# Performance work log

Measured on AMD Instinct MI355X. Metric: run time of the kernel, lower is better.

The kernel has to match this reference:

```python
import jax, jax.numpy as jnp
import numpy as np

ALPHA = 0.2  # LeakyReLU negative slope


def setup_inputs() -> dict:
    key = jax.random.key(0)
    k1, k2, k3, k4 = jax.random.split(key, 4)
    B, N, F_IN, F_OUT = 8, 2048, 512, 256
    h = jax.random.normal(k1, (B, N, F_IN), dtype=jnp.float32)
    # torch nn.Linear weights: [out, in]
    W = jax.random.normal(k2, (F_OUT, F_IN), dtype=jnp.float32) * (1.414 / np.sqrt(F_IN))
    a1 = jax.random.normal(k3, (1, F_OUT), dtype=jnp.float32) * (1.414 / np.sqrt(F_OUT))
    a2 = jax.random.normal(k4, (1, F_OUT), dtype=jnp.float32) * (1.414 / np.sqrt(F_OUT))
    return {"h": h, "W": W, "a1": a1, "a2": a2}


def reference(h, W, a1, a2):
    # Wh: [B, N, F_out]
    Wh = jnp.einsum('bnf,of->bno', h, W)
    # additive attention scores
    s1 = jnp.einsum('bno,o->bn', Wh, a1[0])  # [B, N]
    s2 = jnp.einsum('bno,o->bn', Wh, a2[0])  # [B, N]
    e = s1[:, :, None] + s2[:, None, :]       # [B, N, N]
    e = jnp.where(e > 0, e, ALPHA * e)         # LeakyReLU
    attention = jax.nn.softmax(e, axis=2)      # softmax over last dim
    # dropout p=0.0 -> identity
    h_prime = jnp.einsum('bnm,bmo->bno', attention, Wh)
    return jax.nn.elu(h_prime)  # concat=True path
```

## Files before the change

### kernel.cpp

```cpp
#include <hip/hip_runtime.h>

typedef __attribute__((ext_vector_type(8))) _Float16 half8;
typedef __attribute__((ext_vector_type(4))) _Float16 half4;
typedef __attribute__((ext_vector_type(4))) float f32x4;
#if __has_builtin(__builtin_amdgcn_cvt_pkrtz)
typedef __attribute__((ext_vector_type(2))) __fp16 fp16x2;
#endif

#define ALPHA 0.2f
#define LOG2E 1.44269504f

__device__ __forceinline__ void gload_lds16(const void* g, void* l) {
  __builtin_amdgcn_global_load_lds((const __attribute__((address_space(1))) unsigned int*)g,
                                   (__attribute__((address_space(3))) unsigned int*)l, 16, 0, 0);
}

__device__ __forceinline__ float fexp2(float x) {
#if __has_builtin(__builtin_amdgcn_exp2f)
  return __builtin_amdgcn_exp2f(x);
#else
  return exp2f(x);
#endif
}

__global__ __launch_bounds__(256) void k_convW(const float* __restrict__ W,
                                               _Float16* __restrict__ W16) {
  int idx4 = blockIdx.x * 256 + threadIdx.x;
  int n = idx4 >> 7;
  int q = idx4 & 127;
  float4 v = *reinterpret_cast<const float4*>(W + n * 512 + q * 4);
  half4 hv = {(_Float16)v.x, (_Float16)v.y, (_Float16)v.z, (_Float16)v.w};
  int kp = (q * 4) ^ ((n & 7) << 3);
  *reinterpret_cast<half4*>(W16 + n * 512 + kp) = hv;
}

__global__ __launch_bounds__(256) void k_uvec(const float* __restrict__ W,
                                              const float* __restrict__ a1,
                                              const float* __restrict__ a2,
                                              float* __restrict__ u1,
                                              float* __restrict__ u2) {
  __shared__ float p1[4][64], p2[4][64];
  int t = threadIdx.x;
  int l = t & 63, g = t >> 6;
  int k = blockIdx.x * 64 + l;
  float x1 = 0.f, x2 = 0.f;
  for (int o = g * 64; o < g * 64 + 64; ++o) {
    float wv = W[o * 512 + k];
    x1 += wv * a1[o];
    x2 += wv * a2[o];
  }
  p1[g][l] = x1; p2[g][l] = x2;
  __syncthreads();
  if (g == 0) {
    u1[k] = p1[0][l] + p1[1][l] + p1[2][l] + p1[3][l];
    u2[k] = p2[0][l] + p2[1][l] + p2[2][l] + p2[3][l];
  }
}

__global__ __launch_bounds__(512) void k_gemm_wh(const float* __restrict__ h,
                                                 const _Float16* __restrict__ W16,
                                                 const float* __restrict__ u1,
                                                 const float* __restrict__ u2,
                                                 float* __restrict__ s1o,
                                                 float* __restrict__ s2o,
                                                 _Float16* __restrict__ WhT) {
  __shared__ _Float16 Ab[2][64 * 64];
  __shared__ _Float16 Bb[3][256 * 64];
  __shared__ float u_lds[1024];
  const int t = threadIdx.x, lane = t & 63, w = t >> 6;
  const int rg = w >> 2, cg = w & 3;
  const int i0 = blockIdx.x * 64;
  const int b = i0 >> 11, n0 = i0 & 2047;
  const int ar = t >> 3, au = t & 7;
  const int arow = lane & 15;
  const float* hrow = h + (size_t)(i0 + ar) * 512 + au * 8;
  const int awoff = ar * 128 + ((au * 16) ^ ((ar & 7) << 4));

  u_lds[t] = u1[t];
  u_lds[512 + t] = u2[t];
  __syncthreads();

  f32x4 acc[2][4];
#pragma unroll
  for (int mi = 0; mi < 2; ++mi)
#pragma unroll
    for (int ni = 0; ni < 4; ++ni) acc[mi][ni] = (f32x4){0.f, 0.f, 0.f, 0.f};
  float x1 = 0.f, x2 = 0.f;

  float4 aRx[2], aRy[2];
  aRx[0] = *reinterpret_cast<const float4*>(hrow);
  aRy[0] = *reinterpret_cast<const float4*>(hrow + 4);
#pragma unroll
  for (int x = 0; x < 2; ++x)
#pragma unroll
    for (int q = 0; q < 4; ++q) {
      int idx = q * 512 + t;
      int cl = idx >> 3, uu = idx & 7;
      gload_lds16(W16 + cl * 512 + x * 64 + uu * 8, (char*)&Bb[x][0] + idx * 16);
    }
  aRx[1] = *reinterpret_cast<const float4*>(hrow + 64);
  aRy[1] = *reinterpret_cast<const float4*>(hrow + 68);
  {
    float4 a0 = aRx[0], a1v = aRy[0];
    half8 av;
    av[0] = (_Float16)a0.x; av[1] = (_Float16)a0.y; av[2] = (_Float16)a0.z; av[3] = (_Float16)a0.w;
    av[4] = (_Float16)a1v.x; av[5] = (_Float16)a1v.y; av[6] = (_Float16)a1v.z; av[7] = (_Float16)a1v.w;
    *reinterpret_cast<half8*>((char*)&Ab[0][0] + awoff) = av;
    const float* up1 = &u_lds[au * 8];
    const float* up2 = &u_lds[512 + au * 8];
    x1 += a0.x * up1[0] + a0.y * up1[1] + a0.z * up1[2] + a0.w * up1[3]
        + a1v.x * up1[4] + a1v.y * up1[5] + a1v.z * up1[6] + a1v.w * up1[7];
    x2 += a0.x * up2[0] + a0.y * up2[1] + a0.z * up2[2] + a0.w * up2[3]
        + a1v.x * up2[4] + a1v.y * up2[5] + a1v.z * up2[6] + a1v.w * up2[7];
  }

#pragma unroll
  for (int kt = 0; kt < 8; ++kt) {
    asm volatile("s_waitcnt vmcnt(6) lgkmcnt(0)" ::: "memory");
    __builtin_amdgcn_s_barrier();
    if (kt < 6) {
      const int k0 = (kt + 2) * 64;
      const int p = (kt + 2) % 3;
#pragma unroll
      for (int q = 0; q < 4; ++q) {
        int idx = q * 512 + t;
        int cl = idx >> 3, uu = idx & 7;
        gload_lds16(W16 + cl * 512 + k0 + uu * 8, (char*)&Bb[p][0] + idx * 16);
      }
      aRx[kt & 1] = *reinterpret_cast<const float4*>(hrow + k0);
      aRy[kt & 1] = *reinterpret_cast<const float4*>(hrow + k0 + 4);
    }
    if (kt < 7) {
      float4 a0 = aRx[(kt + 1) & 1], a1v = aRy[(kt + 1) & 1];
      half8 av;
      av[0] = (_Float16)a0.x; av[1] = (_Float16)a0.y; av[2] = (_Float16)a0.z; av[3] = (_Float16)a0.w;
      av[4] = (_Float16)a1v.x; av[5] = (_Float16)a1v.y; av[6] = (_Float16)a1v.z; av[7] = (_Float16)a1v.w;
      *reinterpret_cast<half8*>((char*)&Ab[(kt + 1) & 1][0] + awoff) = av;
      const float* up1 = &u_lds[(kt + 1) * 64 + au * 8];
      const float* up2 = &u_lds[512 + (kt + 1) * 64 + au * 8];
      x1 += a0.x * up1[0] + a0.y * up1[1] + a0.z * up1[2] + a0.w * up1[3]
          + a1v.x * up1[4] + a1v.y * up1[5] + a1v.z * up1[6] + a1v.w * up1[7];
      x2 += a0.x * up2[0] + a0.y * up2[1] + a0.z * up2[2] + a0.w * up2[3]
          + a1v.x * up2[4] + a1v.y * up2[5] + a1v.z * up2[6] + a1v.w * up2[7];
    }
    const char* Ac = (const char*)&Ab[kt & 1][0];
    const char* Bc = (const char*)&Bb[kt % 3][0];
#pragma unroll
    for (int kk = 0; kk < 2; ++kk) {
      const int jb = ((lane >> 4) * 8 + kk * 32) * 2;
      half8 afr[2];
#pragma unroll
      for (int mi = 0; mi < 2; ++mi) {
        int rr = rg * 32 + 16 * mi + arow;
        afr[mi] = *reinterpret_cast<const half8*>(Ac + rr * 128 + (jb ^ ((rr & 7) << 4)));
      }
#pragma unroll
      for (int ni = 0; ni < 4; ++ni) {
        int nn = cg * 64 + 16 * ni + arow;
        half8 bfr = *reinterpret_cast<const half8*>(Bc + nn * 128 + (jb ^ ((nn & 7) << 4)));
#pragma unroll
        for (int mi = 0; mi < 2; ++mi)
          acc[mi][ni] = __builtin_amdgcn_mfma_f32_16x16x32_f16(afr[mi], bfr, acc[mi][ni], 0, 0, 0);
      }
    }
  }
  x1 += __shfl_xor(x1, 1); x1 += __shfl_xor(x1, 2); x1 += __shfl_xor(x1, 4);
  x2 += __shfl_xor(x2, 1); x2 += __shfl_xor(x2, 2); x2 += __shfl_xor(x2, 4);
  if (au == 0) { s1o[i0 + ar] = x1; s2o[i0 + ar] = x2; }
  _Float16* whtb = WhT + (size_t)b * 256 * 2048;
#pragma unroll
  for (int mi = 0; mi < 2; ++mi)
#pragma unroll
    for (int ni = 0; ni < 4; ++ni) {
      int c = cg * 64 + 16 * ni + arow;
      int nb = n0 + rg * 32 + 16 * mi + (lane >> 4) * 4;
      int np = nb ^ ((c & 7) << 3);
      f32x4 a = acc[mi][ni];
      half4 hv = {(_Float16)a[0], (_Float16)a[1], (_Float16)a[2], (_Float16)a[3]};
      *reinterpret_cast<half4*>(whtb + (size_t)c * 2048 + np) = hv;
    }
}

__global__ __launch_bounds__(1024) void k_attn(const _Float16* __restrict__ WhT,
                                               const float* __restrict__ s1,
                                               const float* __restrict__ s2,
                                               float* __restrict__ out) {
  __shared__ _Float16 Bb[3][256 * 64];
  __shared__ _Float16 Pb[2][64 * 64];
  __shared__ float s2s[2048];
  __shared__ float red[16];
  __shared__ float d_lds[64];
  const int t = threadIdx.x, lane = t & 63, w = t >> 6;
  const int rg = w >> 2, cg = w & 3;
  const int b = blockIdx.x & 7;
  const int i0 = (blockIdx.x >> 3) * 64;
  const _Float16* whtb = WhT + (size_t)b * 256 * 2048;
  const int arow = lane & 15;
  const int pr = t >> 4, pj = t & 15;
  const float s1v = s1[b * 2048 + i0 + pr];

  float2 sv2 = *reinterpret_cast<const float2*>(s2 + b * 2048 + t * 2);
  float m0 = fmaxf(sv2.x, sv2.y);
  *reinterpret_cast<float2*>(&s2s[t * 2]) = make_float2(sv2.x * LOG2E, sv2.y * LOG2E);
#pragma unroll
  for (int off = 32; off >= 1; off >>= 1) m0 = fmaxf(m0, __shfl_xor(m0, off));
  if (lane == 0) red[w] = m0;
  __syncthreads();
  float smaxL;
  {
    float mm = red[0];
#pragma unroll
    for (int i = 1; i < 16; ++i) mm = fmaxf(mm, red[i]);
    smaxL = mm * LOG2E;
  }
  const float s1L = LOG2E * s1v;
  const float e0L = s1L + smaxL;
  const float mrowL = fmaxf(e0L, ALPHA * e0L);
  const float C1 = s1L - mrowL;
  const float C2 = fmaf(ALPHA, s1L, -mrowL);
  const int pwoff = pr * 128 + ((pj * 8) ^ ((pr & 7) << 4));
  half8 onesb;
  {
    _Float16 ov = (arow == 0) ? (_Float16)1.0f : (_Float16)0.0f;
#pragma unroll
    for (int x = 0; x < 8; ++x) onesb[x] = ov;
  }
  f32x4 acc[4];
#pragma unroll
  for (int ni = 0; ni < 4; ++ni) acc[ni] = (f32x4){0.f, 0.f, 0.f, 0.f};
  f32x4 accd = (f32x4){0.f, 0.f, 0.f, 0.f};

  {
    float4 sv = *reinterpret_cast<const float4*>(&s2s[pj * 4]);
    float p0 = fexp2(fmaxf(C1 + sv.x, fmaf(ALPHA, sv.x, C2)));
    float p1 = fexp2(fmaxf(C1 + sv.y, fmaf(ALPHA, sv.y, C2)));
    float p2 = fexp2(fmaxf(C1 + sv.z, fmaf(ALPHA, sv.z, C2)));
    float p3 = fexp2(fmaxf(C1 + sv.w, fmaf(ALPHA, sv.w, C2)));
    half4 hv;
#if __has_builtin(__builtin_amdgcn_cvt_pkrtz)
    fp16x2 q0 = __builtin_amdgcn_cvt_pkrtz(p0, p1);
    fp16x2 q1 = __builtin_amdgcn_cvt_pkrtz(p2, p3);
    hv[0] = (_Float16)q0[0]; hv[1] = (_Float16)q0[1];
    hv[2] = (_Float16)q1[0]; hv[3] = (_Float16)q1[1];
#else
    hv[0] = (_Float16)p0; hv[1] = (_Float16)p1; hv[2] = (_Float16)p2; hv[3] = (_Float16)p3;
#endif
    *reinterpret_cast<half4*>((char*)&Pb[0][0] + pwoff) = hv;
  }
#pragma unroll
  for (int x = 0; x < 2; ++x)
#pragma unroll
    for (int q = 0; q < 2; ++q) {
      int idx = q * 1024 + t;
      int cl = idx >> 3, uu = idx & 7;
      gload_lds16(whtb + (size_t)cl * 2048 + x * 64 + uu * 8, (char*)&Bb[x][0] + idx * 16);
    }

  for (int jt = 0; jt < 32; ++jt) {
    if (jt < 31) asm volatile("s_waitcnt vmcnt(2) lgkmcnt(0)" ::: "memory");
    else         asm volatile("s_waitcnt vmcnt(0) lgkmcnt(0)" ::: "memory");
    __builtin_amdgcn_s_barrier();
    if (jt < 30) {
      const int j0n = (jt + 2) * 64;
      const int p = (jt + 2) % 3;
#pragma unroll
      for (int q = 0; q < 2; ++q) {
        int idx = q * 1024 + t;
        int cl = idx >> 3, uu = idx & 7;
        gload_lds16(whtb + (size_t)cl * 2048 + j0n + uu * 8, (char*)&Bb[p][0] + idx * 16);
      }
    }
    if (jt < 31) {
      float4 sv = *reinterpret_cast<const float4*>(&s2s[(jt + 1) * 64 + pj * 4]);
      float p0 = fexp2(fmaxf(C1 + sv.x, fmaf(ALPHA, sv.x, C2)));
      float p1 = fexp2(fmaxf(C1 + sv.y, fmaf(ALPHA, sv.y, C2)));
      float p2 = fexp2(fmaxf(C1 + sv.z, fmaf(ALPHA, sv.z, C2)));
      float p3 = fexp2(fmaxf(C1 + sv.w, fmaf(ALPHA, sv.w, C2)));
      half4 hv;
#if __has_builtin(__builtin_amdgcn_cvt_pkrtz)
      fp16x2 q0 = __builtin_amdgcn_cvt_pkrtz(p0, p1);
      fp16x2 q1 = __builtin_amdgcn_cvt_pkrtz(p2, p3);
      hv[0] = (_Float16)q0[0]; hv[1] = (_Float16)q0[1];
      hv[2] = (_Float16)q1[0]; hv[3] = (_Float16)q1[1];
#else
      hv[0] = (_Float16)p0; hv[1] = (_Float16)p1; hv[2] = (_Float16)p2; hv[3] = (_Float16)p3;
#endif
      *reinterpret_cast<half4*>((char*)&Pb[(jt + 1) & 1][0] + pwoff) = hv;
    }
    const char* Bc = (const char*)&Bb[jt % 3][0];
    const char* Pc = (const char*)&Pb[jt & 1][0];
#pragma unroll
    for (int kk = 0; kk < 2; ++kk) {
      const int jb = ((lane >> 4) * 8 + kk * 32) * 2;
      const int ar64 = rg * 16 + arow;
      half8 afr = *reinterpret_cast<const half8*>(Pc + ar64 * 128 + (jb ^ ((ar64 & 7) << 4)));
      if (cg == 0)
        accd = __builtin_amdgcn_mfma_f32_16x16x32_f16(afr, onesb, accd, 0, 0, 0);
#pragma unroll
      for (int ni = 0; ni < 4; ++ni) {
        int cl = cg * 64 + 16 * ni + arow;
        half8 bfr = *reinterpret_cast<const half8*>(Bc + cl * 128 + (jb ^ ((cl & 7) << 4)));
        acc[ni] = __builtin_amdgcn_mfma_f32_16x16x32_f16(afr, bfr, acc[ni], 0, 0, 0);
      }
    }
  }
  if (cg == 0 && arow == 0) {
#pragma unroll
    for (int reg = 0; reg < 4; ++reg)
      d_lds[rg * 16 + (lane >> 4) * 4 + reg] = accd[reg];
  }
  __syncthreads();
  const size_t ob = ((size_t)b * 2048 + i0 + rg * 16) * 256 + cg * 64;
#pragma unroll
  for (int reg = 0; reg < 4; ++reg) {
    int rr = (lane >> 4) * 4 + reg;
    float inv = 1.0f / d_lds[rg * 16 + rr];
#pragma unroll
    for (int ni = 0; ni < 4; ++ni) {
      int c = 16 * ni + arow;
      float v = acc[ni][reg] * inv;
      v = v > 0.f ? v : (__expf(v) - 1.f);
      out[ob + (size_t)rr * 256 + c] = v;
    }
  }
}

extern "C" void kernel_launch(void* const* d_in, const int* in_sizes, int n_in,
                              void* d_out, int out_size, void* d_ws, size_t ws_size,
                              hipStream_t stream) {
  (void)in_sizes; (void)n_in; (void)out_size; (void)ws_size;
  const float* h = (const float*)d_in[0];
  const float* W = (const float*)d_in[1];
  const float* a1 = (const float*)d_in[2];
  const float* a2 = (const float*)d_in[3];
  float* out = (float*)d_out;
  char* ws = (char*)d_ws;
  _Float16* WhT = (_Float16*)(ws);
  _Float16* W16 = (_Float16*)(ws + 8388608);
  float* u1 = (float*)(ws + 8650752);
  float* u2 = (float*)(ws + 8652800);
  float* s1 = (float*)(ws + 8654848);
  float* s2 = (float*)(ws + 8720384);

  hipLaunchKernelGGL(k_convW, dim3(128), dim3(256), 0, stream, W, W16);
  hipLaunchKernelGGL(k_uvec, dim3(8), dim3(256), 0, stream, W, a1, a2, u1, u2);
  hipLaunchKernelGGL(k_gemm_wh, dim3(256), dim3(512), 0, stream, h, W16, u1, u2, s1, s2, WhT);
  hipLaunchKernelGGL(k_attn, dim3(256), dim3(1024), 0, stream, WhT, s1, s2, out);
}
```

Before: 71.85 us.

## Shrink Wh GEMM tile to 32 rows with 256 threads and double-buffered W

The Wh projection kernel now processes 32 rows per block with 4 waves instead of 64 rows with 8 waves, and launches twice as many blocks. The W tile pipeline goes from a triple buffer with two tiles of prefetch to a simple double buffer with one-ahead prefetch and a plain __syncthreads per step. The u vectors are now read directly from global memory instead of being staged in LDS. The aim is more blocks, less LDS per block, and better occupancy across CUs, at the cost of reloading W from L2 twice as often and having less latency hiding in the pipeline.

```diff
diff --git a/kernel.cpp b/kernel.cpp
--- a/kernel.cpp
+++ b/kernel.cpp
@@ -57,106 +57,83 @@
   }
 }
 
-__global__ __launch_bounds__(512) void k_gemm_wh(const float* __restrict__ h,
+__global__ __launch_bounds__(256) void k_gemm_wh(const float* __restrict__ h,
                                                  const _Float16* __restrict__ W16,
                                                  const float* __restrict__ u1,
                                                  const float* __restrict__ u2,
                                                  float* __restrict__ s1o,
                                                  float* __restrict__ s2o,
                                                  _Float16* __restrict__ WhT) {
-  __shared__ _Float16 Ab[2][64 * 64];
-  __shared__ _Float16 Bb[3][256 * 64];
-  __shared__ float u_lds[1024];
+  __shared__ _Float16 Ab[2][32 * 64];
+  __shared__ _Float16 Bb[2][256 * 64];
   const int t = threadIdx.x, lane = t & 63, w = t >> 6;
-  const int rg = w >> 2, cg = w & 3;
-  const int i0 = blockIdx.x * 64;
+  const int i0 = blockIdx.x * 32;
   const int b = i0 >> 11, n0 = i0 & 2047;
   const int ar = t >> 3, au = t & 7;
-  const int arow = lane & 15;
   const float* hrow = h + (size_t)(i0 + ar) * 512 + au * 8;
-  const int awoff = ar * 128 + ((au * 16) ^ ((ar & 7) << 4));
-
-  u_lds[t] = u1[t];
-  u_lds[512 + t] = u2[t];
-  __syncthreads();
 
   f32x4 acc[2][4];
 #pragma unroll
   for (int mi = 0; mi < 2; ++mi)
 #pragma unroll
     for (int ni = 0; ni < 4; ++ni) acc[mi][ni] = (f32x4){0.f, 0.f, 0.f, 0.f};
+
+  float4 aR0 = *reinterpret_cast<const float4*>(hrow);
+  float4 aR1 = *reinterpret_cast<const float4*>(hrow + 4);
+#pragma unroll
+  for (int q = 0; q < 8; ++q) {
+    int idx = (q * 4 + w) * 64 + lane;
+    int nn = idx >> 3, uu = idx & 7;
+    gload_lds16(W16 + nn * 512 + uu * 8, (char*)&Bb[0][0] + idx * 16);
+  }
   float x1 = 0.f, x2 = 0.f;
 
-  float4 aRx[2], aRy[2];
-  aRx[0] = *reinterpret_cast<const float4*>(hrow);
-  aRy[0] = *reinterpret_cast<const float4*>(hrow + 4);
-#pragma unroll
-  for (int x = 0; x < 2; ++x)
-#pragma unroll
-    for (int q = 0; q < 4; ++q) {
-      int idx = q * 512 + t;
-      int cl = idx >> 3, uu = idx & 7;
-      gload_lds16(W16 + cl * 512 + x * 64 + uu * 8, (char*)&Bb[x][0] + idx * 16);
-    }
-  aRx[1] = *reinterpret_cast<const float4*>(hrow + 64);
-  aRy[1] = *reinterpret_cast<const float4*>(hrow + 68);
-  {
-    float4 a0 = aRx[0], a1v = aRy[0];
-    half8 av;
-    av[0] = (_Float16)a0.x; av[1] = (_Float16)a0.y; av[2] = (_Float16)a0.z; av[3] = (_Float16)a0.w;
-    av[4] = (_Float16)a1v.x; av[5] = (_Float16)a1v.y; av[6] = (_Float16)a1v.z; av[7] = (_Float16)a1v.w;
-    *reinterpret_cast<half8*>((char*)&Ab[0][0] + awoff) = av;
-    const float* up1 = &u_lds[au * 8];
-    const float* up2 = &u_lds[512 + au * 8];
-    x1 += a0.x * up1[0] + a0.y * up1[1] + a0.z * up1[2] + a0.w * up1[3]
-        + a1v.x * up1[4] + a1v.y * up1[5] + a1v.z * up1[6] + a1v.w * up1[7];
-    x2 += a0.x * up2[0] + a0.y * up2[1] + a0.z * up2[2] + a0.w * up2[3]
-        + a1v.x * up2[4] + a1v.y * up2[5] + a1v.z * up2[6] + a1v.w * up2[7];
-  }
-
-#pragma unroll
   for (int kt = 0; kt < 8; ++kt) {
-    asm volatile("s_waitcnt vmcnt(6) lgkmcnt(0)" ::: "memory");
-    __builtin_amdgcn_s_barrier();
-    if (kt < 6) {
-      const int k0 = (kt + 2) * 64;
-      const int p = (kt + 2) % 3;
-#pragma unroll
-      for (int q = 0; q < 4; ++q) {
-        int idx = q * 512 + t;
-        int cl = idx >> 3, uu = idx & 7;
-        gload_lds16(W16 + cl * 512 + k0 + uu * 8, (char*)&Bb[p][0] + idx * 16);
-      }
-      aRx[kt & 1] = *reinterpret_cast<const float4*>(hrow + k0);
-      aRy[kt & 1] = *reinterpret_cast<const float4*>(hrow + k0 + 4);
-    }
+    const int cur = kt & 1;
+    {
+      half8 av;
+      av[0] = (_Float16)aR0.x; av[1] = (_Float16)aR0.y;
+      av[2] = (_Float16)aR0.z; av[3] = (_Float16)aR0.w;
+      av[4] = (_Float16)aR1.x; av[5] = (_Float16)aR1.y;
+      av[6] = (_Float16)aR1.z; av[7] = (_Float16)aR1.w;
+      *reinterpret_cast<half8*>((char*)&Ab[cur][0] + ar * 128 + ((au * 16) ^ ((ar & 7) << 4))) = av;
+      const float* up1 = u1 + kt * 64 + au * 8;
+      const float* up2 = u2 + kt * 64 + au * 8;
+      float4 u1a = *reinterpret_cast<const float4*>(up1);
+      float4 u1b = *reinterpret_cast<const float4*>(up1 + 4);
+      float4 u2a = *reinterpret_cast<const float4*>(up2);
+      float4 u2b = *reinterpret_cast<const float4*>(up2 + 4);
+      x1 += aR0.x * u1a.x + aR0.y * u1a.y + aR0.z * u1a.z + aR0.w * u1a.w
+          + aR1.x * u1b.x + aR1.y * u1b.y + aR1.z * u1b.z + aR1.w * u1b.w;
+      x2 += aR0.x * u2a.x + aR0.y * u2a.y + aR0.z * u2a.z + aR0.w * u2a.w
+          + aR1.x * u2b.x + aR1.y * u2b.y + aR1.z * u2b.z + aR1.w * u2b.w;
+    }
+    __syncthreads();
     if (kt < 7) {
-      float4 a0 = aRx[(kt + 1) & 1], a1v = aRy[(kt + 1) & 1];
-      half8 av;
-      av[0] = (_Float16)a0.x; av[1] = (_Float16)a0.y; av[2] = (_Float16)a0.z; av[3] = (_Float16)a0.w;
-      av[4] = (_Float16)a1v.x; av[5] = (_Float16)a1v.y; av[6] = (_Float16)a1v.z; av[7] = (_Float16)a1v.w;
-      *reinterpret_cast<half8*>((char*)&Ab[(kt + 1) & 1][0] + awoff) = av;
-      const float* up1 = &u_lds[(kt + 1) * 64 + au * 8];
-      const float* up2 = &u_lds[512 + (kt + 1) * 64 + au * 8];
-      x1 += a0.x * up1[0] + a0.y * up1[1] + a0.z * up1[2] + a0.w * up1[3]
-          + a1v.x * up1[4] + a1v.y * up1[5] + a1v.z * up1[6] + a1v.w * up1[7];
-      x2 += a0.x * up2[0] + a0.y * up2[1] + a0.z * up2[2] + a0.w * up2[3]
-          + a1v.x * up2[4] + a1v.y * up2[5] + a1v.z * up2[6] + a1v.w * up2[7];
-    }
-    const char* Ac = (const char*)&Ab[kt & 1][0];
-    const char* Bc = (const char*)&Bb[kt % 3][0];
+      const int k0 = (kt + 1) * 64;
+      aR0 = *reinterpret_cast<const float4*>(hrow + k0);
+      aR1 = *reinterpret_cast<const float4*>(hrow + k0 + 4);
+#pragma unroll
+      for (int q = 0; q < 8; ++q) {
+        int idx = (q * 4 + w) * 64 + lane;
+        int nn = idx >> 3, uu = idx & 7;
+        gload_lds16(W16 + nn * 512 + k0 + uu * 8, (char*)&Bb[cur ^ 1][0] + idx * 16);
+      }
+    }
+    const char* Ac = (const char*)&Ab[cur][0];
+    const char* Bc = (const char*)&Bb[cur][0];
 #pragma unroll
     for (int kk = 0; kk < 2; ++kk) {
-      const int jb = ((lane >> 4) * 8 + kk * 32) * 2;
+      const int jb = (lane >> 4) * 16 + kk * 64;
       half8 afr[2];
 #pragma unroll
       for (int mi = 0; mi < 2; ++mi) {
-        int rr = rg * 32 + 16 * mi + arow;
+        int rr = (lane & 15) + 16 * mi;
         afr[mi] = *reinterpret_cast<const half8*>(Ac + rr * 128 + (jb ^ ((rr & 7) << 4)));
       }
 #pragma unroll
       for (int ni = 0; ni < 4; ++ni) {
-        int nn = cg * 64 + 16 * ni + arow;
+        int nn = 64 * w + 16 * ni + (lane & 15);
         half8 bfr = *reinterpret_cast<const half8*>(Bc + nn * 128 + (jb ^ ((nn & 7) << 4)));
 #pragma unroll
         for (int mi = 0; mi < 2; ++mi)
@@ -172,8 +149,8 @@
   for (int mi = 0; mi < 2; ++mi)
 #pragma unroll
     for (int ni = 0; ni < 4; ++ni) {
-      int c = cg * 64 + 16 * ni + arow;
-      int nb = n0 + rg * 32 + 16 * mi + (lane >> 4) * 4;
+      int c = 64 * w + 16 * ni + (lane & 15);
+      int nb = n0 + 16 * mi + (lane >> 4) * 4;
       int np = nb ^ ((c & 7) << 3);
       f32x4 a = acc[mi][ni];
       half4 hv = {(_Float16)a[0], (_Float16)a[1], (_Float16)a[2], (_Float16)a[3]};
@@ -344,6 +321,6 @@
 
   hipLaunchKernelGGL(k_convW, dim3(128), dim3(256), 0, stream, W, W16);
   hipLaunchKernelGGL(k_uvec, dim3(8), dim3(256), 0, stream, W, a1, a2, u1, u2);
-  hipLaunchKernelGGL(k_gemm_wh, dim3(256), dim3(512), 0, stream, h, W16, u1, u2, s1, s2, WhT);
+  hipLaunchKernelGGL(k_gemm_wh, dim3(512), dim3(256), 0, stream, h, W16, u1, u2, s1, s2, WhT);
   hipLaunchKernelGGL(k_attn, dim3(256), dim3(1024), 0, stream, WhT, s1, s2, out);
 }
```

After: 72.66 us. About the same (+1.1%).
